# Performance work log

Hardware: AMD Instinct MI355X
Metric: run time of the kernel (lower is better)

The kernel has to match this reference:

```python
import jax, jax.numpy as jnp
import numpy as np

N = 100000
NFEAT = 128
NHID = 16
HEADS = 8
NCLASS = 40
E = 1600000
NEG_SLOPE = 0.2  # PyG GATConv default


def glorot(key, shape):
    fan = shape[0] + shape[-1]
    limit = float(np.sqrt(6.0 / fan))
    return jax.random.uniform(key, shape, jnp.float32, -limit, limit)


def setup_inputs() -> dict:
    key = jax.random.key(0)
    ks = jax.random.split(key, 10)
    x = jax.random.normal(ks[0], (N, NFEAT), jnp.float32)
    adj = jnp.zeros((1,), jnp.float32)  # unused by forward, kept for signature parity
    edge_index = jax.random.randint(ks[1], (2, E), 0, N, jnp.int64)
    # layer 1: GATConv(NFEAT, NHID, heads=HEADS)
    W1 = glorot(ks[2], (NFEAT, HEADS * NHID))
    att_src1 = glorot(ks[3], (HEADS, NHID))
    att_dst1 = glorot(ks[4], (HEADS, NHID))
    b1 = jnp.zeros((HEADS * NHID,), jnp.float32)
    # layer 2: GATConv(HEADS*NHID, NCLASS, heads=1)
    W2 = glorot(ks[5], (HEADS * NHID, NCLASS))
    att_src2 = glorot(ks[6], (1, NCLASS))
    att_dst2 = glorot(ks[7], (1, NCLASS))
    b2 = jnp.zeros((NCLASS,), jnp.float32)
    return {"x": x, "adj": adj, "edge_index": edge_index,
            "W1": W1, "att_src1": att_src1, "att_dst1": att_dst1, "b1": b1,
            "W2": W2, "att_src2": att_src2, "att_dst2": att_dst2, "b2": b2}


def gat_conv(x, W, att_src, att_dst, bias, src, dst, heads, out_ch):
    n = x.shape[0]
    h = (x @ W).reshape(n, heads, out_ch)              # [N,H,C]
    a_src = (h * att_src[None]).sum(-1)                # [N,H]
    a_dst = (h * att_dst[None]).sum(-1)                # [N,H]
    e = jax.nn.leaky_relu(a_src[src] + a_dst[dst], NEG_SLOPE)  # [E,H]
    # softmax over incoming edges of each destination node
    m = jax.ops.segment_max(e, dst, num_segments=n)
    e = jnp.exp(e - m[dst])
    s = jax.ops.segment_sum(e, dst, num_segments=n)
    alpha = e / s[dst]                                  # [E,H]
    msg = h[src] * alpha[:, :, None]                    # [E,H,C]
    out = jax.ops.segment_sum(msg, dst, num_segments=n)  # [N,H,C]
    return out.reshape(n, heads * out_ch) + bias


def reference(x, adj, edge_index, W1, att_src1, att_dst1, b1, W2, att_src2, att_dst2, b2):
    # PyG GATConv adds self-loops by default
    loops = jnp.arange(N, dtype=edge_index.dtype)
    src = jnp.concatenate([edge_index[0], loops])
    dst = jnp.concatenate([edge_index[1], loops])
    # eval mode: F.dropout is identity
    h = jax.nn.elu(gat_conv(x, W1, att_src1, att_dst1, b1, src, dst, HEADS, NHID))
    h = jax.nn.elu(gat_conv(h, W2, att_src2, att_dst2, b2, src, dst, 1, NCLASS))
    return jax.nn.log_softmax(h, axis=1)
```

## Files before the change

kernel.cpp:

```cpp
#include <hip/hip_runtime.h>

#define NEG_SLOPE 0.2f

__device__ __forceinline__ float lrelu(float v) { return v >= 0.f ? v : NEG_SLOPE * v; }
__device__ __forceinline__ float elu(float v) { return v > 0.f ? v : expm1f(v); }
__device__ __forceinline__ void fma4(float4& a, float s, const float4 b) {
    a.x += s * b.x; a.y += s * b.y; a.z += s * b.z; a.w += s * b.w;
}
__device__ __forceinline__ unsigned short f2bf(float f) {
    unsigned u = __float_as_uint(f);
    return (unsigned short)((u + 0x7fffu + ((u >> 16) & 1u)) >> 16);
}
__device__ __forceinline__ float bflo(unsigned w) { return __uint_as_float(w << 16); }
__device__ __forceinline__ float bfhi(unsigned w) { return __uint_as_float(w & 0xffff0000u); }
__device__ __forceinline__ float pexp(float v) { return __expf(lrelu(v)); }


__global__ void zero_deg_kernel(int* __restrict__ deg, int n) {
    int t = blockIdx.x * blockDim.x + threadIdx.x;
    if (t < n) deg[t] = 0;
}

__global__ void hist_kernel(const int* __restrict__ ei, int* __restrict__ deg,
                            int* __restrict__ rank, int E, int n) {
    int e = blockIdx.x * blockDim.x + threadIdx.x;
    if (e >= E) return;
    int s = ei[e], d = ei[E + e];
    int r = -1;
    if ((unsigned)s < (unsigned)n && (unsigned)d < (unsigned)n)
        r = atomicAdd(&deg[d], 1);
    rank[e] = r;
}

#define SCAN_T 256
#define SCAN_TILE 1024

__global__ __launch_bounds__(SCAN_T) void scan_p1_kernel(const int* __restrict__ deg,
                                                         int* __restrict__ bsum, int n) {
    __shared__ int red[SCAN_T];
    int t = threadIdx.x;
    int base = blockIdx.x * SCAN_TILE + t * 4;
    int s = 0;
    #pragma unroll
    for (int i = 0; i < 4; i++) {
        int idx = base + i;
        if (idx < n) s += deg[idx];
    }
    red[t] = s;
    __syncthreads();
    for (int off = SCAN_T / 2; off; off >>= 1) {
        if (t < off) red[t] += red[t + off];
        __syncthreads();
    }
    if (t == 0) bsum[blockIdx.x] = red[0];
}

__global__ __launch_bounds__(1024) void scan_p2_kernel(int* __restrict__ bsum, int nb,
                                                       int* __restrict__ total) {
    __shared__ int sh[1024];
    int t = threadIdx.x;
    int v = (t < nb) ? bsum[t] : 0;
    sh[t] = v;
    __syncthreads();
    for (int off = 1; off < 1024; off <<= 1) {
        int add = (t >= off) ? sh[t - off] : 0;
        __syncthreads();
        sh[t] += add;
        __syncthreads();
    }
    if (t < nb) bsum[t] = sh[t] - v;
    if (t == nb - 1) *total = sh[t];
}

__global__ __launch_bounds__(SCAN_T) void scan_p3_kernel(const int* __restrict__ deg,
                                                         const int* __restrict__ bsum,
                                                         int* __restrict__ row_ptr, int n) {
    __shared__ int red[SCAN_T];
    int t = threadIdx.x;
    int base = blockIdx.x * SCAN_TILE + t * 4;
    int v[4];
    int s = 0;
    #pragma unroll
    for (int i = 0; i < 4; i++) {
        int idx = base + i;
        v[i] = (idx < n) ? deg[idx] : 0;
        s += v[i];
    }
    red[t] = s;
    __syncthreads();
    for (int off = 1; off < SCAN_T; off <<= 1) {
        int add = (t >= off) ? red[t - off] : 0;
        __syncthreads();
        red[t] += add;
        __syncthreads();
    }
    int excl = red[t] - s + bsum[blockIdx.x];
    #pragma unroll
    for (int i = 0; i < 4; i++) {
        int idx = base + i;
        if (idx < n) row_ptr[idx] = excl;
        excl += v[i];
    }
}

__global__ void scatter_kernel(const int* __restrict__ ei, const int* __restrict__ rank,
                               const int* __restrict__ row_ptr,
                               int* __restrict__ csr_src, int E, int n) {
    int e = blockIdx.x * blockDim.x + threadIdx.x;
    if (e >= E) return;
    int r = rank[e];
    if (r < 0) return;
    int s = ei[e], d = ei[E + e];
    csr_src[row_ptr[d] + r] = s;
}


__global__ __launch_bounds__(256, 4) void gemm1_kernel(const float* __restrict__ x,
                                                       const float* __restrict__ W1,
                                                       const float* __restrict__ as1,
                                                       const float* __restrict__ ad1,
                                                       unsigned short* __restrict__ h1bf,
                                                       float* __restrict__ a1s,
                                                       float* __restrict__ a1d, int n) {
    __shared__ float Ws[64 * 128];
    __shared__ float xs[32][128];
    const int tid = threadIdx.x;
    const int cg = tid & 31;
    const int ng = tid >> 5;
    const int base = blockIdx.x * 32;

    #pragma unroll 1
    for (int q = tid; q < 32 * 32; q += 256) {
        int nn = q >> 5, c4 = q & 31;
        int node = base + nn;
        float4 v = make_float4(0.f, 0.f, 0.f, 0.f);
        if (node < n) v = *(const float4*)&x[(size_t)node * 128 + c4 * 4];
        *(float4*)&xs[nn][c4 * 4] = v;
    }

    float4 acc[4];
    #pragma unroll
    for (int mm = 0; mm < 4; mm++) acc[mm] = make_float4(0.f, 0.f, 0.f, 0.f);

    for (int kt = 0; kt < 2; kt++) {
        __syncthreads();
        #pragma unroll 1
        for (int q = tid; q < 64 * 32; q += 256) {
            int row = q >> 5, c4 = q & 31;
            *(float4*)&Ws[row * 128 + c4 * 4] =
                *(const float4*)&W1[(size_t)(kt * 64 + row) * 128 + c4 * 4];
        }
        __syncthreads();
        #pragma unroll 2
        for (int k4 = 0; k4 < 64; k4 += 4) {
            float4 xv[4];
            #pragma unroll
            for (int mm = 0; mm < 4; mm++)
                xv[mm] = *(const float4*)&xs[ng * 4 + mm][kt * 64 + k4];
            #pragma unroll
            for (int k = 0; k < 4; k++) {
                float4 w = *(const float4*)&Ws[(k4 + k) * 128 + cg * 4];
                #pragma unroll
                for (int mm = 0; mm < 4; mm++) {
                    float xk = (k == 0) ? xv[mm].x : (k == 1) ? xv[mm].y
                             : (k == 2) ? xv[mm].z : xv[mm].w;
                    fma4(acc[mm], xk, w);
                }
            }
        }
    }
    float4 av = *(const float4*)&as1[cg * 4];
    float4 dv = *(const float4*)&ad1[cg * 4];
    #pragma unroll
    for (int mm = 0; mm < 4; mm++) {
        int node = base + ng * 4 + mm;
        if (node < n) {
            ushort4 hb;
            hb.x = f2bf(acc[mm].x); hb.y = f2bf(acc[mm].y);
            hb.z = f2bf(acc[mm].z); hb.w = f2bf(acc[mm].w);
            *(ushort4*)&h1bf[(size_t)node * 128 + cg * 4] = hb;
        }
        float p = acc[mm].x * av.x + acc[mm].y * av.y + acc[mm].z * av.z + acc[mm].w * av.w;
        p += __shfl_xor(p, 1);
        p += __shfl_xor(p, 2);
        float q = acc[mm].x * dv.x + acc[mm].y * dv.y + acc[mm].z * dv.z + acc[mm].w * dv.w;
        q += __shfl_xor(q, 1);
        q += __shfl_xor(q, 2);
        if ((cg & 3) == 0 && node < n) {
            a1s[node * 8 + (cg >> 2)] = p;
            a1d[node * 8 + (cg >> 2)] = q;
        }
    }
}

__global__ __launch_bounds__(256) void agg1_kernel(const int* __restrict__ row_ptr,
                                                   const int* __restrict__ csr_src,
                                                   const float* __restrict__ a1s,
                                                   const float* __restrict__ a1d,
                                                   const uint4* __restrict__ h1q,
                                                   const float* __restrict__ b1,
                                                   float* __restrict__ h2, int n) {
    int lane = threadIdx.x & 63;
    int d = blockIdx.x * 4 + (threadIdx.x >> 6);
    if (d >= n) return;
    const int g = lane >> 4;
    const int q = lane & 15;
    const int h = q >> 1;
    const float adh = a1d[d * 8 + h];

    float acc[8];
    #pragma unroll
    for (int i = 0; i < 8; i++) acc[i] = 0.f;
    float sum = 0.f;
    if (g == 0) {
        uint4 w = h1q[(size_t)d * 16 + q];
        float ps = pexp(a1s[d * 8 + h] + adh);
        acc[0] = ps * bflo(w.x); acc[1] = ps * bfhi(w.x);
        acc[2] = ps * bflo(w.y); acc[3] = ps * bfhi(w.y);
        acc[4] = ps * bflo(w.z); acc[5] = ps * bfhi(w.z);
        acc[6] = ps * bflo(w.w); acc[7] = ps * bfhi(w.w);
        sum = ps;
    }
    int beg = row_ptr[d], end = row_ptr[d + 1];
    for (int e = beg + g; e < end; e += 4) {
        int s = csr_src[e];
        uint4 w = h1q[(size_t)s * 16 + q];
        float p = pexp(a1s[s * 8 + h] + adh);
        acc[0] += p * bflo(w.x); acc[1] += p * bfhi(w.x);
        acc[2] += p * bflo(w.y); acc[3] += p * bfhi(w.y);
        acc[4] += p * bflo(w.z); acc[5] += p * bfhi(w.z);
        acc[6] += p * bflo(w.w); acc[7] += p * bfhi(w.w);
        sum += p;
    }
    sum += __shfl_xor(sum, 16); sum += __shfl_xor(sum, 32);
    #pragma unroll
    for (int i = 0; i < 8; i++) {
        acc[i] += __shfl_xor(acc[i], 16);
        acc[i] += __shfl_xor(acc[i], 32);
    }
    if (g == 0) {
        float rs = 1.f / sum;
        float4 b0 = *(const float4*)&b1[8 * q];
        float4 b4 = *(const float4*)&b1[8 * q + 4];
        float4 o0, o1;
        o0.x = elu(acc[0] * rs + b0.x); o0.y = elu(acc[1] * rs + b0.y);
        o0.z = elu(acc[2] * rs + b0.z); o0.w = elu(acc[3] * rs + b0.w);
        o1.x = elu(acc[4] * rs + b4.x); o1.y = elu(acc[5] * rs + b4.y);
        o1.z = elu(acc[6] * rs + b4.z); o1.w = elu(acc[7] * rs + b4.w);
        *(float4*)&h2[(size_t)d * 128 + 8 * q] = o0;
        *(float4*)&h2[(size_t)d * 128 + 8 * q + 4] = o1;
    }
}


#define WT_STRIDE 136
__global__ __launch_bounds__(320, 4) void gemm2_kernel(const float* __restrict__ h2,
                                                       const float* __restrict__ W2,
                                                       float* __restrict__ h3f,
                                                       unsigned short* __restrict__ h3bf,
                                                       int n) {
    __shared__ float WsT[40 * WT_STRIDE];
    __shared__ float xs[64][128];
    const int tid = threadIdx.x;
    const int j = tid % 40;
    const int no = tid / 40;
    const int base = blockIdx.x * 64;

    #pragma unroll 1
    for (int i = tid; i < 128 * 40; i += 320) {
        int k = i / 40, jj = i % 40;
        WsT[jj * WT_STRIDE + k] = W2[i];
    }
    #pragma unroll 1
    for (int q = tid; q < 64 * 32; q += 320) {
        int nn = q >> 5, c4 = q & 31;
        int node = base + nn;
        float4 v = make_float4(0.f, 0.f, 0.f, 0.f);
        if (node < n) v = *(const float4*)&h2[(size_t)node * 128 + c4 * 4];
        *(float4*)&xs[nn][c4 * 4] = v;
    }
    __syncthreads();

    float acc[8];
    #pragma unroll
    for (int m = 0; m < 8; m++) acc[m] = 0.f;
    #pragma unroll 4
    for (int k4 = 0; k4 < 128; k4 += 4) {
        float4 wv = *(const float4*)&WsT[j * WT_STRIDE + k4];
        #pragma unroll
        for (int m = 0; m < 8; m++) {
            float4 xv = *(const float4*)&xs[no + m * 8][k4];
            acc[m] += xv.x * wv.x + xv.y * wv.y + xv.z * wv.z + xv.w * wv.w;
        }
    }
    #pragma unroll
    for (int m = 0; m < 8; m++) {
        int node = base + no + m * 8;
        if (node < n) {
            h3f[(size_t)node * 40 + j] = acc[m];
            h3bf[(size_t)node * 40 + j] = f2bf(acc[m]);
        }
    }
}

__global__ void attn2s_kernel(const float* __restrict__ h3f, const float* __restrict__ as2,
                              float* __restrict__ a2s, int n) {
    int t = blockIdx.x * blockDim.x + threadIdx.x;
    if (t >= n) return;
    const float* row = &h3f[(size_t)t * 40];
    float ss = 0.f;
    #pragma unroll
    for (int c = 0; c < 40; c++) ss += row[c] * as2[c];
    a2s[t] = ss;
}

__global__ __launch_bounds__(256) void agg2_final_kernel(const int* __restrict__ row_ptr,
                                                         const int* __restrict__ csr_src,
                                                         const float* __restrict__ a2s,
                                                         const float* __restrict__ ad2,
                                                         const float* __restrict__ h3f,
                                                         const unsigned* __restrict__ h3p,
                                                         const float* __restrict__ b2,
                                                         float* __restrict__ out, int n) {
    int lane = threadIdx.x & 63;
    int d = blockIdx.x * 4 + (threadIdx.x >> 6);
    if (d >= n) return;
    const int g = lane >> 5;
    const int q = lane & 31;
    const bool act = (q < 20);

    float2 hv = make_float2(0.f, 0.f);
    if (act && g == 0) hv = *(const float2*)&h3f[(size_t)d * 40 + 2 * q];
    float p = (act && g == 0) ? (hv.x * ad2[2 * q] + hv.y * ad2[2 * q + 1]) : 0.f;
    #pragma unroll
    for (int off = 32; off; off >>= 1) p += __shfl_xor(p, off, 64);
    const float adh = p;

    float acc0 = 0.f, acc1 = 0.f, sum = 0.f;
    if (g == 0) {
        float ps = pexp(a2s[d] + adh);
        acc0 = ps * hv.x; acc1 = ps * hv.y; sum = ps;
    }
    int beg = row_ptr[d], end = row_ptr[d + 1];
    int e = beg + g;
    for (; e + 6 < end; e += 8) {
        int s0 = csr_src[e],     s1 = csr_src[e + 2];
        int s2 = csr_src[e + 4], s3 = csr_src[e + 6];
        float a0 = a2s[s0], a1 = a2s[s1], a2 = a2s[s2], a3 = a2s[s3];
        unsigned w0 = 0u, w1 = 0u, w2 = 0u, w3 = 0u;
        if (act) {
            w0 = h3p[(size_t)s0 * 20 + q]; w1 = h3p[(size_t)s1 * 20 + q];
            w2 = h3p[(size_t)s2 * 20 + q]; w3 = h3p[(size_t)s3 * 20 + q];
        }
        float p0 = pexp(a0 + adh), p1 = pexp(a1 + adh);
        float p2 = pexp(a2 + adh), p3 = pexp(a3 + adh);
        acc0 += p0 * bflo(w0) + p1 * bflo(w1) + p2 * bflo(w2) + p3 * bflo(w3);
        acc1 += p0 * bfhi(w0) + p1 * bfhi(w1) + p2 * bfhi(w2) + p3 * bfhi(w3);
        sum += (p0 + p1) + (p2 + p3);
    }
    for (; e < end; e += 2) {
        int s = csr_src[e];
        float pe = pexp(a2s[s] + adh);
        unsigned w = act ? h3p[(size_t)s * 20 + q] : 0u;
        acc0 += pe * bflo(w);
        acc1 += pe * bfhi(w);
        sum += pe;
    }
    sum += __shfl_xor(sum, 32);
    acc0 += __shfl_xor(acc0, 32);
    acc1 += __shfl_xor(acc1, 32);

    float rs = 1.f / sum;
    float v0 = -3.0e38f, v1 = -3.0e38f;
    if (act) {
        v0 = elu(acc0 * rs + b2[2 * q]);
        v1 = elu(acc1 * rs + b2[2 * q + 1]);
    }
    float mx = (act && g == 0) ? fmaxf(v0, v1) : -3.0e38f;
    #pragma unroll
    for (int off = 32; off; off >>= 1) mx = fmaxf(mx, __shfl_xor(mx, off, 64));
    float es = (act && g == 0) ? (__expf(v0 - mx) + __expf(v1 - mx)) : 0.f;
    #pragma unroll
    for (int off = 32; off; off >>= 1) es += __shfl_xor(es, off, 64);
    if (act && g == 0) {
        float ls = logf(es);
        float2 o;
        o.x = v0 - mx - ls;
        o.y = v1 - mx - ls;
        *(float2*)&out[(size_t)d * 40 + 2 * q] = o;
    }
}

extern "C" void kernel_launch(void* const* d_in, const int* in_sizes, int n_in,
                              void* d_out, int out_size, void* d_ws, size_t ws_size,
                              hipStream_t stream) {
    const float* x   = (const float*)d_in[0];
    const int*   ei  = (const int*)d_in[2];
    const float* W1  = (const float*)d_in[3];
    const float* as1 = (const float*)d_in[4];
    const float* ad1 = (const float*)d_in[5];
    const float* b1  = (const float*)d_in[6];
    const float* W2  = (const float*)d_in[7];
    const float* as2 = (const float*)d_in[8];
    const float* ad2 = (const float*)d_in[9];
    const float* b2  = (const float*)d_in[10];
    float* out = (float*)d_out;

    const int n = in_sizes[0] / 128;
    const int E = in_sizes[2] / 2;
    const int nb = (n + SCAN_TILE - 1) / SCAN_TILE;

    float* ws = (float*)d_ws;
    unsigned short* h1bf = (unsigned short*)ws;
    float* h2 = ws + (size_t)n * 64;
    float* A  = h2 + (size_t)n * 128;
    int* deg    = (int*)A;
    int* bsum   = deg + n;
    float* a1s  = A;
    float* a1d  = A + (size_t)n * 8;
    float* a2s  = A;
    int* row_ptr = (int*)(A + (size_t)n * 16);
    int* csr_src = row_ptr + (n + 1);
    int* rank    = csr_src + E;
    unsigned short* h3bf = h1bf;
    float* h3f = ws + (size_t)n * 20;

    zero_deg_kernel<<<(n + 255) / 256, 256, 0, stream>>>(deg, n);
    hist_kernel<<<(E + 255) / 256, 256, 0, stream>>>(ei, deg, rank, E, n);
    scan_p1_kernel<<<nb, SCAN_T, 0, stream>>>(deg, bsum, n);
    scan_p2_kernel<<<1, 1024, 0, stream>>>(bsum, nb, &row_ptr[n]);
    scan_p3_kernel<<<nb, SCAN_T, 0, stream>>>(deg, bsum, row_ptr, n);
    scatter_kernel<<<(E + 255) / 256, 256, 0, stream>>>(ei, rank, row_ptr, csr_src, E, n);

    gemm1_kernel<<<(n + 31) / 32, 256, 0, stream>>>(x, W1, as1, ad1, h1bf, a1s, a1d, n);
    agg1_kernel<<<(n + 3) / 4, 256, 0, stream>>>(row_ptr, csr_src, a1s, a1d,
                                                 (const uint4*)h1bf, b1, h2, n);

    gemm2_kernel<<<(n + 63) / 64, 320, 0, stream>>>(h2, W2, h3f, h3bf, n);
    attn2s_kernel<<<(n + 255) / 256, 256, 0, stream>>>(h3f, as2, a2s, n);
    agg2_final_kernel<<<(n + 3) / 4, 256, 0, stream>>>(row_ptr, csr_src, a2s, ad2, h3f,
                                                       (const unsigned*)h3bf, b2, out, n);
}
```

Before: 509.0 us.

## Use fp16 MFMA for layer-1 GEMM and switch intermediate storage to fp16

Replaces the scalar-FMA layer-1 GEMM with a matrix-core kernel using mfma_f32_16x16x32_f16. It reads a pre-transposed fp16 copy of W1 from swizzled LDS and converts x to fp16 in registers. Intermediate features h1 and h3 are now stored as fp16 instead of bf16, and the aggregation kernels decode them accordingly. The layer-2 destination attention score is computed once per node in the attn2 kernel rather than via a wave reduction inside agg2. This cuts GEMM compute cost at the price of an extra transpose kernel launch and fp16 rounding of inputs, with some overflow risk.

```diff
diff --git a/kernel.cpp b/kernel.cpp
--- a/kernel.cpp
+++ b/kernel.cpp
@@ -1,19 +1,21 @@
 #include <hip/hip_runtime.h>
+#include <stdint.h>
 
 #define NEG_SLOPE 0.2f
 
 __device__ __forceinline__ float lrelu(float v) { return v >= 0.f ? v : NEG_SLOPE * v; }
 __device__ __forceinline__ float elu(float v) { return v > 0.f ? v : expm1f(v); }
-__device__ __forceinline__ void fma4(float4& a, float s, const float4 b) {
-    a.x += s * b.x; a.y += s * b.y; a.z += s * b.z; a.w += s * b.w;
-}
-__device__ __forceinline__ unsigned short f2bf(float f) {
-    unsigned u = __float_as_uint(f);
-    return (unsigned short)((u + 0x7fffu + ((u >> 16) & 1u)) >> 16);
-}
-__device__ __forceinline__ float bflo(unsigned w) { return __uint_as_float(w << 16); }
-__device__ __forceinline__ float bfhi(unsigned w) { return __uint_as_float(w & 0xffff0000u); }
 __device__ __forceinline__ float pexp(float v) { return __expf(lrelu(v)); }
+
+typedef _Float16 h16x2 __attribute__((ext_vector_type(2)));
+typedef _Float16 half8 __attribute__((ext_vector_type(8)));
+typedef float floatx4 __attribute__((ext_vector_type(4)));
+
+__device__ __forceinline__ void fma_h2(float& a0, float& a1, float p, unsigned u) {
+    h16x2 h = __builtin_bit_cast(h16x2, u);
+    a0 += p * (float)h[0];
+    a1 += p * (float)h[1];
+}
 
 
 __global__ void zero_deg_kernel(int* __restrict__ deg, int n) {
@@ -115,80 +117,74 @@
 }
 
 
-__global__ __launch_bounds__(256, 4) void gemm1_kernel(const float* __restrict__ x,
-                                                       const float* __restrict__ W1,
-                                                       const float* __restrict__ as1,
-                                                       const float* __restrict__ ad1,
-                                                       unsigned short* __restrict__ h1bf,
-                                                       float* __restrict__ a1s,
-                                                       float* __restrict__ a1d, int n) {
-    __shared__ float Ws[64 * 128];
-    __shared__ float xs[32][128];
+__global__ void w1t_kernel(const float* __restrict__ W1, _Float16* __restrict__ w1t) {
+    int t = blockIdx.x * 256 + threadIdx.x;
+    int col = t >> 7, k = t & 127;
+    w1t[col * 128 + k] = (_Float16)W1[k * 128 + col];
+}
+
+__global__ __launch_bounds__(256) void gemm1_mfma_kernel(
+    const float* __restrict__ x, const _Float16* __restrict__ w1t,
+    const float* __restrict__ as1, const float* __restrict__ ad1,
+    _Float16* __restrict__ h1h, float* __restrict__ a1s, float* __restrict__ a1d, int n) {
+    __shared__ __align__(16) char Wl[32768];
     const int tid = threadIdx.x;
-    const int cg = tid & 31;
-    const int ng = tid >> 5;
-    const int base = blockIdx.x * 32;
-
-    #pragma unroll 1
-    for (int q = tid; q < 32 * 32; q += 256) {
-        int nn = q >> 5, c4 = q & 31;
-        int node = base + nn;
-        float4 v = make_float4(0.f, 0.f, 0.f, 0.f);
-        if (node < n) v = *(const float4*)&x[(size_t)node * 128 + c4 * 4];
-        *(float4*)&xs[nn][c4 * 4] = v;
-    }
-
-    float4 acc[4];
-    #pragma unroll
-    for (int mm = 0; mm < 4; mm++) acc[mm] = make_float4(0.f, 0.f, 0.f, 0.f);
-
-    for (int kt = 0; kt < 2; kt++) {
-        __syncthreads();
-        #pragma unroll 1
-        for (int q = tid; q < 64 * 32; q += 256) {
-            int row = q >> 5, c4 = q & 31;
-            *(float4*)&Ws[row * 128 + c4 * 4] =
-                *(const float4*)&W1[(size_t)(kt * 64 + row) * 128 + c4 * 4];
-        }
-        __syncthreads();
-        #pragma unroll 2
-        for (int k4 = 0; k4 < 64; k4 += 4) {
-            float4 xv[4];
-            #pragma unroll
-            for (int mm = 0; mm < 4; mm++)
-                xv[mm] = *(const float4*)&xs[ng * 4 + mm][kt * 64 + k4];
-            #pragma unroll
-            for (int k = 0; k < 4; k++) {
-                float4 w = *(const float4*)&Ws[(k4 + k) * 128 + cg * 4];
-                #pragma unroll
-                for (int mm = 0; mm < 4; mm++) {
-                    float xk = (k == 0) ? xv[mm].x : (k == 1) ? xv[mm].y
-                             : (k == 2) ? xv[mm].z : xv[mm].w;
-                    fma4(acc[mm], xk, w);
-                }
+    {
+        const uint4* Wg = (const uint4*)w1t;
+        #pragma unroll
+        for (int i = 0; i < 8; i++) {
+            int it = tid + i * 256;
+            uint4 v = Wg[it];
+            int b = it * 16;
+            *(uint4*)&Wl[b ^ (((b >> 8) & 7) << 4)] = v;
+        }
+    }
+    const int wave = tid >> 6, lane = tid & 63;
+    const int cl = lane & 15, g = lane >> 4;
+    const int wbase = blockIdx.x * 64 + wave * 16;
+
+    int arow = wbase + cl;
+    if (arow >= n) arow = n - 1;
+    half8 afr[4];
+    #pragma unroll
+    for (int t = 0; t < 4; t++) {
+        const float4 v0 = *(const float4*)&x[(size_t)arow * 128 + 32 * t + g * 8];
+        const float4 v1 = *(const float4*)&x[(size_t)arow * 128 + 32 * t + g * 8 + 4];
+        afr[t][0] = (_Float16)v0.x; afr[t][1] = (_Float16)v0.y;
+        afr[t][2] = (_Float16)v0.z; afr[t][3] = (_Float16)v0.w;
+        afr[t][4] = (_Float16)v1.x; afr[t][5] = (_Float16)v1.y;
+        afr[t][6] = (_Float16)v1.z; afr[t][7] = (_Float16)v1.w;
+    }
+    __syncthreads();
+
+    #pragma unroll
+    for (int ct = 0; ct < 8; ct++) {
+        const int col = ct * 16 + cl;
+        half8 bfr[4];
+        #pragma unroll
+        for (int t = 0; t < 4; t++) {
+            int b = (col << 8) + 64 * t + 16 * g;
+            bfr[t] = *(half8*)&Wl[b ^ ((col & 7) << 4)];
+        }
+        floatx4 acc = {0.f, 0.f, 0.f, 0.f};
+        #pragma unroll
+        for (int t = 0; t < 4; t++)
+            acc = __builtin_amdgcn_mfma_f32_16x16x32_f16(afr[t], bfr[t], acc, 0, 0, 0);
+        const float av = as1[col], dv = ad1[col];
+        #pragma unroll
+        for (int i = 0; i < 4; i++) {
+            int r = wbase + g * 4 + i;
+            float hv = acc[i];
+            if (r < n) h1h[(size_t)r * 128 + col] = (_Float16)hv;
+            float ps = hv * av, pd = hv * dv;
+            ps += __shfl_xor(ps, 1); ps += __shfl_xor(ps, 2);
+            ps += __shfl_xor(ps, 4); ps += __shfl_xor(ps, 8);
+            pd += __shfl_xor(pd, 1); pd += __shfl_xor(pd, 2);
+            pd += __shfl_xor(pd, 4); pd += __shfl_xor(pd, 8);
+            if (cl == 0 && r < n) {
+                a1s[r * 8 + ct] = ps;
+                a1d[r * 8 + ct] = pd;
             }
-        }
-    }
-    float4 av = *(const float4*)&as1[cg * 4];
-    float4 dv = *(const float4*)&ad1[cg * 4];
-    #pragma unroll
-    for (int mm = 0; mm < 4; mm++) {
-        int node = base + ng * 4 + mm;
-        if (node < n) {
-            ushort4 hb;
-            hb.x = f2bf(acc[mm].x); hb.y = f2bf(acc[mm].y);
-            hb.z = f2bf(acc[mm].z); hb.w = f2bf(acc[mm].w);
-            *(ushort4*)&h1bf[(size_t)node * 128 + cg * 4] = hb;
-        }
-        float p = acc[mm].x * av.x + acc[mm].y * av.y + acc[mm].z * av.z + acc[mm].w * av.w;
-        p += __shfl_xor(p, 1);
-        p += __shfl_xor(p, 2);
-        float q = acc[mm].x * dv.x + acc[mm].y * dv.y + acc[mm].z * dv.z + acc[mm].w * dv.w;
-        q += __shfl_xor(q, 1);
-        q += __shfl_xor(q, 2);
-        if ((cg & 3) == 0 && node < n) {
-            a1s[node * 8 + (cg >> 2)] = p;
-            a1d[node * 8 + (cg >> 2)] = q;
         }
     }
 }
@@ -215,10 +211,10 @@
     if (g == 0) {
         uint4 w = h1q[(size_t)d * 16 + q];
         float ps = pexp(a1s[d * 8 + h] + adh);
-        acc[0] = ps * bflo(w.x); acc[1] = ps * bfhi(w.x);
-        acc[2] = ps * bflo(w.y); acc[3] = ps * bfhi(w.y);
-        acc[4] = ps * bflo(w.z); acc[5] = ps * bfhi(w.z);
-        acc[6] = ps * bflo(w.w); acc[7] = ps * bfhi(w.w);
+        fma_h2(acc[0], acc[1], ps, w.x);
+        fma_h2(acc[2], acc[3], ps, w.y);
+        fma_h2(acc[4], acc[5], ps, w.z);
+        fma_h2(acc[6], acc[7], ps, w.w);
         sum = ps;
     }
     int beg = row_ptr[d], end = row_ptr[d + 1];
@@ -226,10 +222,10 @@
         int s = csr_src[e];
         uint4 w = h1q[(size_t)s * 16 + q];
         float p = pexp(a1s[s * 8 + h] + adh);
-        acc[0] += p * bflo(w.x); acc[1] += p * bfhi(w.x);
-        acc[2] += p * bflo(w.y); acc[3] += p * bfhi(w.y);
-        acc[4] += p * bflo(w.z); acc[5] += p * bfhi(w.z);
-        acc[6] += p * bflo(w.w); acc[7] += p * bfhi(w.w);
+        fma_h2(acc[0], acc[1], p, w.x);
+        fma_h2(acc[2], acc[3], p, w.y);
+        fma_h2(acc[4], acc[5], p, w.z);
+        fma_h2(acc[6], acc[7], p, w.w);
         sum += p;
     }
     sum += __shfl_xor(sum, 16); sum += __shfl_xor(sum, 32);
@@ -257,7 +253,7 @@
 __global__ __launch_bounds__(320, 4) void gemm2_kernel(const float* __restrict__ h2,
                                                        const float* __restrict__ W2,
                                                        float* __restrict__ h3f,
-                                                       unsigned short* __restrict__ h3bf,
+                                                       _Float16* __restrict__ h3h,
                                                        int n) {
     __shared__ float WsT[40 * WT_STRIDE];
     __shared__ float xs[64][128];
@@ -298,26 +294,32 @@
         int node = base + no + m * 8;
         if (node < n) {
             h3f[(size_t)node * 40 + j] = acc[m];
-            h3bf[(size_t)node * 40 + j] = f2bf(acc[m]);
-        }
-    }
-}
-
-__global__ void attn2s_kernel(const float* __restrict__ h3f, const float* __restrict__ as2,
-                              float* __restrict__ a2s, int n) {
+            h3h[(size_t)node * 40 + j] = (_Float16)acc[m];
+        }
+    }
+}
+
+__global__ void attn2_kernel(const float* __restrict__ h3f, const float* __restrict__ as2,
+                             const float* __restrict__ ad2,
+                             float* __restrict__ a2s, float* __restrict__ a2d, int n) {
     int t = blockIdx.x * blockDim.x + threadIdx.x;
     if (t >= n) return;
     const float* row = &h3f[(size_t)t * 40];
-    float ss = 0.f;
-    #pragma unroll
-    for (int c = 0; c < 40; c++) ss += row[c] * as2[c];
+    float ss = 0.f, dd = 0.f;
+    #pragma unroll
+    for (int c = 0; c < 40; c++) {
+        float v = row[c];
+        ss += v * as2[c];
+        dd += v * ad2[c];
+    }
     a2s[t] = ss;
+    a2d[t] = dd;
 }
 
 __global__ __launch_bounds__(256) void agg2_final_kernel(const int* __restrict__ row_ptr,
                                                          const int* __restrict__ csr_src,
                                                          const float* __restrict__ a2s,
-                                                         const float* __restrict__ ad2,
+                                                         const float* __restrict__ a2d,
                                                          const float* __restrict__ h3f,
                                                          const unsigned* __restrict__ h3p,
                                                          const float* __restrict__ b2,
@@ -331,10 +333,7 @@
 
     float2 hv = make_float2(0.f, 0.f);
     if (act && g == 0) hv = *(const float2*)&h3f[(size_t)d * 40 + 2 * q];
-    float p = (act && g == 0) ? (hv.x * ad2[2 * q] + hv.y * ad2[2 * q + 1]) : 0.f;
-    #pragma unroll
-    for (int off = 32; off; off >>= 1) p += __shfl_xor(p, off, 64);
-    const float adh = p;
+    const float adh = a2d[d];
 
     float acc0 = 0.f, acc1 = 0.f, sum = 0.f;
     if (g == 0) {
@@ -354,16 +353,17 @@
         }
         float p0 = pexp(a0 + adh), p1 = pexp(a1 + adh);
         float p2 = pexp(a2 + adh), p3 = pexp(a3 + adh);
-        acc0 += p0 * bflo(w0) + p1 * bflo(w1) + p2 * bflo(w2) + p3 * bflo(w3);
-        acc1 += p0 * bfhi(w0) + p1 * bfhi(w1) + p2 * bfhi(w2) + p3 * bfhi(w3);
+        fma_h2(acc0, acc1, p0, w0);
+        fma_h2(acc0, acc1, p1, w1);
+        fma_h2(acc0, acc1, p2, w2);
+        fma_h2(acc0, acc1, p3, w3);
         sum += (p0 + p1) + (p2 + p3);
     }
     for (; e < end; e += 2) {
         int s = csr_src[e];
         float pe = pexp(a2s[s] + adh);
         unsigned w = act ? h3p[(size_t)s * 20 + q] : 0u;
-        acc0 += pe * bflo(w);
-        acc1 += pe * bfhi(w);
+        fma_h2(acc0, acc1, pe, w);
         sum += pe;
     }
     sum += __shfl_xor(sum, 32);
@@ -411,7 +411,7 @@
     const int nb = (n + SCAN_TILE - 1) / SCAN_TILE;
 
     float* ws = (float*)d_ws;
-    unsigned short* h1bf = (unsigned short*)ws;
+    _Float16* h1h = (_Float16*)ws;
     float* h2 = ws + (size_t)n * 64;
     float* A  = h2 + (size_t)n * 128;
     int* deg    = (int*)A;
@@ -419,12 +419,15 @@
     float* a1s  = A;
     float* a1d  = A + (size_t)n * 8;
     float* a2s  = A;
+    float* a2d  = A + (size_t)n;
     int* row_ptr = (int*)(A + (size_t)n * 16);
     int* csr_src = row_ptr + (n + 1);
     int* rank    = csr_src + E;
-    unsigned short* h3bf = h1bf;
+    _Float16* w1t = (_Float16*)(((uintptr_t)(rank + E) + 63) & ~(uintptr_t)63);
+    _Float16* h3h = h1h;
     float* h3f = ws + (size_t)n * 20;
 
+    w1t_kernel<<<64, 256, 0, stream>>>(W1, w1t);
     zero_deg_kernel<<<(n + 255) / 256, 256, 0, stream>>>(deg, n);
     hist_kernel<<<(E + 255) / 256, 256, 0, stream>>>(ei, deg, rank, E, n);
     scan_p1_kernel<<<nb, SCAN_T, 0, stream>>>(deg, bsum, n);
@@ -432,12 +435,12 @@
     scan_p3_kernel<<<nb, SCAN_T, 0, stream>>>(deg, bsum, row_ptr, n);
     scatter_kernel<<<(E + 255) / 256, 256, 0, stream>>>(ei, rank, row_ptr, csr_src, E, n);
 
-    gemm1_kernel<<<(n + 31) / 32, 256, 0, stream>>>(x, W1, as1, ad1, h1bf, a1s, a1d, n);
+    gemm1_mfma_kernel<<<(n + 63) / 64, 256, 0, stream>>>(x, w1t, as1, ad1, h1h, a1s, a1d, n);
     agg1_kernel<<<(n + 3) / 4, 256, 0, stream>>>(row_ptr, csr_src, a1s, a1d,
-                                                 (const uint4*)h1bf, b1, h2, n);
-
-    gemm2_kernel<<<(n + 63) / 64, 320, 0, stream>>>(h2, W2, h3f, h3bf, n);
-    attn2s_kernel<<<(n + 255) / 256, 256, 0, stream>>>(h3f, as2, a2s, n);
-    agg2_final_kernel<<<(n + 3) / 4, 256, 0, stream>>>(row_ptr, csr_src, a2s, ad2, h3f,
-                                                       (const unsigned*)h3bf, b2, out, n);
-}
+                                                 (const uint4*)h1h, b1, h2, n);
+
+    gemm2_kernel<<<(n + 63) / 64, 320, 0, stream>>>(h2, W2, h3f, h3h, n);
+    attn2_kernel<<<(n + 255) / 256, 256, 0, stream>>>(h3f, as2, ad2, a2s, a2d, n);
+    agg2_final_kernel<<<(n + 3) / 4, 256, 0, stream>>>(row_ptr, csr_src, a2s, a2d, h3f,
+                                                       (const unsigned*)h3h, b2, out, n);
+}
```

Measured after the change: 485.5 us. 1.05x faster.
